# Kernel optimization log

Hardware: AMD Instinct MI355X
Metric: run time of the kernel (lower is better)

Reference implementation:

```python
import jax, jax.numpy as jnp
import numpy as np

B, D, E, K, NC, NH = 8192, 1280, 4, 2, 20, 4
CD = D // NC      # chunk_dim = 64
HD = CD // NH     # head_dim = 16
FF = CD * 4       # ffn hidden = 256
EPS = 1e-8


def setup_inputs() -> dict:
    key = jax.random.key(0)
    ks = jax.random.split(key, 12)
    f = lambda k, sh, s=0.02: jax.random.normal(k, sh, jnp.float32) * s
    return {
        "x": jax.random.normal(ks[0], (B, D), jnp.float32),
        "gate_w1": f(ks[1], (E * 4, D)), "gate_b1": jnp.zeros((E * 4,), jnp.float32),
        "gate_w2": f(ks[2], (E, E * 4)), "gate_b2": jnp.zeros((E,), jnp.float32),
        "pos_embed": f(ks[3], (E, NC, CD)),
        "norm1_g": jnp.ones((E, CD), jnp.float32),
        "in_proj_w": f(ks[4], (E, 3 * CD, CD)), "in_proj_b": jnp.zeros((E, 3 * CD), jnp.float32),
        "out_proj_w": f(ks[5], (E, CD, CD)), "out_proj_b": jnp.zeros((E, CD), jnp.float32),
        "ls1_g": jnp.full((E, CD), 1e-4, jnp.float32),
        "norm2_g": jnp.ones((E, CD), jnp.float32),
        "ffn_w1": f(ks[6], (E, FF, CD)), "ffn_b1": jnp.zeros((E, FF), jnp.float32),
        "ffn_w2": f(ks[7], (E, CD, FF)), "ffn_b2": jnp.zeros((E, CD), jnp.float32),
        "ls2_g": jnp.full((E, CD), 1e-4, jnp.float32),
        "proj_w": f(ks[8], (E, D, D)), "proj_b": jnp.zeros((E, D), jnp.float32),
    }


def _rms(v, g):
    # torch RMSNorm in source: x / (||x||_2 * dim^-0.5 + eps) * g
    n = jnp.linalg.norm(v, axis=-1, keepdims=True) * (CD ** -0.5)
    return v / (n + EPS) * g


def _expert(x, pos, n1g, ipw, ipb, opw, opb, l1, n2g, fw1, fb1, fw2, fb2, l2, pw, pb):
    b = x.shape[0]
    xs = x.reshape(b, NC, CD) + pos            # [b, NC, CD]
    xn = _rms(xs, n1g)
    qkv = xn @ ipw.T + ipb                      # [b, NC, 3*CD]
    q, k, v = jnp.split(qkv, 3, axis=-1)
    q = q.reshape(b, NC, NH, HD).transpose(0, 2, 1, 3)
    k = k.reshape(b, NC, NH, HD).transpose(0, 2, 1, 3)
    v = v.reshape(b, NC, NH, HD).transpose(0, 2, 1, 3)
    att = jax.nn.softmax(jnp.einsum('bhqd,bhkd->bhqk', q, k) * (HD ** -0.5), axis=-1)
    o = jnp.einsum('bhqk,bhkd->bhqd', att, v).transpose(0, 2, 1, 3).reshape(b, NC, CD)
    o = o @ opw.T + opb
    xs = xs + l1 * o                            # residual + LayerScale
    h = jax.nn.relu(_rms(xs, n2g) @ fw1.T + fb1) @ fw2.T + fb2
    xs = xs + l2 * h
    return xs.reshape(b, D) @ pw.T + pb         # final proj [b, D]


def reference(x, gate_w1, gate_b1, gate_w2, gate_b2, pos_embed, norm1_g,
              in_proj_w, in_proj_b, out_proj_w, out_proj_b, ls1_g, norm2_g,
              ffn_w1, ffn_b1, ffn_w2, ffn_b2, ls2_g, proj_w, proj_b):
    logits = jnp.tanh(x @ gate_w1.T + gate_b1) @ gate_w2.T + gate_b2   # [B, E]
    scores = jax.nn.softmax(logits, axis=-1)
    tk_s, tk_i = jax.lax.top_k(scores, K)
    tk_s = tk_s / (tk_s.sum(-1, keepdims=True) + 1e-6)
    onehot = jax.nn.one_hot(tk_i, E, dtype=x.dtype)                    # [B, K, E]
    w = (onehot * tk_s[..., None]).sum(1)                              # [B, E] combine weights
    eout = jax.vmap(_expert, in_axes=(None,) + (0,) * 15)(
        x, pos_embed, norm1_g, in_proj_w, in_proj_b, out_proj_w, out_proj_b,
        ls1_g, norm2_g, ffn_w1, ffn_b1, ffn_w2, ffn_b2, ls2_g, proj_w, proj_b)  # [E, B, D]
    output = jnp.einsum('ebd,be->bd', eout, w)
    aux_loss = jnp.float32(0.0)  # eval mode
    load = onehot.sum((0, 1))    # [E]
    return output, aux_loss, load
```

## Files before the change

### kernel.cpp

```cpp
#include <hip/hip_runtime.h>
#include <hip/hip_bf16.h>
#include <math.h>

#define B_SZ 8192
#define D_SZ 1280
#define NE   4
#define NC   20
#define CD   64
#define NH   4
#define HD   16
#define FF   256

typedef __attribute__((ext_vector_type(8))) short bf16x8;
typedef __attribute__((ext_vector_type(4))) float f32x4;

#define WS_TOPI   256
#define WS_TOPW   (WS_TOPI + 2*B_SZ*4)
#define WS_IDX    (WS_TOPW + 2*B_SZ*4)
#define WS_WGT    (WS_IDX  + 2*B_SZ*4)
#define WS_ER0    (WS_WGT  + 2*B_SZ*4)
#define WS_ER1    (WS_ER0  + B_SZ*4)
#define WS_PRK    (WS_ER1  + B_SZ*4)
#define WS_BBE    (WS_PRK  + B_SZ*4)
#define WS_BBP    (WS_BBE  + 32*4*4)
#define WS_PRA    (WS_BBP  + 32*16*4)
#define WS_PRB    (WS_PRA  + (B_SZ+128)*4)
#define WS_PW1    (WS_PRB  + (B_SZ+128)*4)
#define WS_PW2    (WS_PW1  + (B_SZ+128)*4)
#define WS_PRW    (WS_PW2  + (B_SZ+128)*4)
#define WS_XSF    532480
#define XSF_ROWS  (2*B_SZ + 128)
#define WS_PWB    (WS_XSF + (size_t)XSF_ROWS * D_SZ * 2)
#define WS_IPWB   (WS_PWB  + (size_t)NE * D_SZ * D_SZ * 2)
#define WS_OPWB   (WS_IPWB + (size_t)NE * 192 * 64 * 2)
#define WS_FW1B   (WS_OPWB + (size_t)NE * 64 * 64 * 2)
#define WS_FW2B   (WS_FW1B + (size_t)NE * 256 * 64 * 2)

__global__ __launch_bounds__(256) void convert_pw(const float* __restrict__ pw,
                                                  __hip_bfloat16* __restrict__ pwb)
{
    size_t i = ((size_t)blockIdx.x * 256 + threadIdx.x) * 8;
    float4 a = *(const float4*)(pw + i);
    float4 b = *(const float4*)(pw + i + 4);
    __hip_bfloat16 h[8];
    h[0] = __float2bfloat16(a.x); h[1] = __float2bfloat16(a.y);
    h[2] = __float2bfloat16(a.z); h[3] = __float2bfloat16(a.w);
    h[4] = __float2bfloat16(b.x); h[5] = __float2bfloat16(b.y);
    h[6] = __float2bfloat16(b.z); h[7] = __float2bfloat16(b.w);
    *(uint4*)(pwb + i) = *(uint4*)h;
}

#define N_IPW (NE*192*64)
#define N_OPW (NE*64*64)
#define N_FW1 (NE*256*64)
#define N_FW2 (NE*64*256)
__global__ __launch_bounds__(256) void convert_small(
    const float* __restrict__ ipw, const float* __restrict__ opw,
    const float* __restrict__ fw1, const float* __restrict__ fw2,
    __hip_bfloat16* __restrict__ ipwb, __hip_bfloat16* __restrict__ opwb,
    __hip_bfloat16* __restrict__ fw1b, __hip_bfloat16* __restrict__ fw2b)
{
    size_t i = ((size_t)blockIdx.x * 256 + threadIdx.x) * 8;
    const float* src; __hip_bfloat16* dst; size_t off;
    if (i < N_IPW)                       { src = ipw; dst = ipwb; off = i; }
    else if (i < N_IPW + N_OPW)          { src = opw; dst = opwb; off = i - N_IPW; }
    else if (i < N_IPW + N_OPW + N_FW1)  { src = fw1; dst = fw1b; off = i - N_IPW - N_OPW; }
    else                                 { src = fw2; dst = fw2b; off = i - N_IPW - N_OPW - N_FW1; }
    float4 a = *(const float4*)(src + off);
    float4 b = *(const float4*)(src + off + 4);
    __hip_bfloat16 h[8];
    h[0] = __float2bfloat16(a.x); h[1] = __float2bfloat16(a.y);
    h[2] = __float2bfloat16(a.z); h[3] = __float2bfloat16(a.w);
    h[4] = __float2bfloat16(b.x); h[5] = __float2bfloat16(b.y);
    h[6] = __float2bfloat16(b.z); h[7] = __float2bfloat16(b.w);
    *(uint4*)(dst + off) = *(uint4*)h;
}

__global__ __launch_bounds__(64) void gate_kernel(
    const float* __restrict__ x, const float* __restrict__ gw1, const float* __restrict__ gb1,
    const float* __restrict__ gw2, const float* __restrict__ gb2,
    int* __restrict__ topi, float* __restrict__ topw)
{
    const int b = blockIdx.x;
    const int lane = threadIdx.x;
    float acc[16];
#pragma unroll
    for (int j = 0; j < 16; ++j) acc[j] = 0.f;
    const float* xr = x + (size_t)b * D_SZ;
    for (int t = 0; t < NC; ++t) {
        float xv = xr[t * 64 + lane];
#pragma unroll
        for (int j = 0; j < 16; ++j) acc[j] += xv * gw1[j * D_SZ + t * 64 + lane];
    }
#pragma unroll
    for (int j = 0; j < 16; ++j) {
        acc[j] += __shfl_xor(acc[j], 32, 64);
        acc[j] += __shfl_xor(acc[j], 16, 64);
        acc[j] += __shfl_xor(acc[j], 8, 64);
        acc[j] += __shfl_xor(acc[j], 4, 64);
        acc[j] += __shfl_xor(acc[j], 2, 64);
        acc[j] += __shfl_xor(acc[j], 1, 64);
    }
    if (lane == 0) {
        float h[16];
#pragma unroll
        for (int j = 0; j < 16; ++j) h[j] = tanhf(acc[j] + gb1[j]);
        float l[4];
#pragma unroll
        for (int e = 0; e < 4; ++e) {
            float sv = gb2[e];
#pragma unroll
            for (int j = 0; j < 16; ++j) sv += h[j] * gw2[e * 16 + j];
            l[e] = sv;
        }
        float m = fmaxf(fmaxf(l[0], l[1]), fmaxf(l[2], l[3]));
        float p[4];
        float sum = 0.f;
#pragma unroll
        for (int e = 0; e < 4; ++e) { p[e] = expf(l[e] - m); sum += p[e]; }
#pragma unroll
        for (int e = 0; e < 4; ++e) p[e] /= sum;
        int i1 = 0;
#pragma unroll
        for (int e = 1; e < 4; ++e) if (p[e] > p[i1]) i1 = e;
        int i2 = (i1 == 0) ? 1 : 0;
#pragma unroll
        for (int e = 0; e < 4; ++e) if (e != i1 && p[e] > p[i2]) i2 = e;
        float s1 = p[i1], s2 = p[i2];
        float denom = s1 + s2 + 1e-6f;
        topi[b * 2 + 0] = i1;
        topi[b * 2 + 1] = i2;
        topw[b * 2 + 0] = s1 / denom;
        topw[b * 2 + 1] = s2 / denom;
    }
}

__global__ __launch_bounds__(256) void count_kernel(
    const int* __restrict__ topi,
    int* __restrict__ cnt, int* __restrict__ pcnt,
    int* __restrict__ er0, int* __restrict__ er1, int* __restrict__ prk,
    int* __restrict__ bbe, int* __restrict__ bbp)
{
    __shared__ int he[4], hp[16];
    const int t = threadIdx.x;
    const int blk = blockIdx.x;
    const int b = blk * 256 + t;
    if (t < 4) he[t] = 0;
    if (t < 16) hp[t] = 0;
    __syncthreads();
    int e0 = topi[b * 2], e1 = topi[b * 2 + 1];
    er0[b] = atomicAdd(&he[e0], 1);
    er1[b] = atomicAdd(&he[e1], 1);
    prk[b] = atomicAdd(&hp[e0 * 4 + e1], 1);
    __syncthreads();
    if (t < 4)  bbe[blk * 4 + t]  = atomicAdd(&cnt[t], he[t]);
    if (t < 16) bbp[blk * 16 + t] = atomicAdd(&pcnt[t], hp[t]);
}

__global__ void offsets_kernel(const int* __restrict__ cnt, const int* __restrict__ pcnt,
                               int* __restrict__ offA, int* __restrict__ poff,
                               float* __restrict__ load_out)
{
    if (threadIdx.x == 0 && blockIdx.x == 0) {
        int a = 0;
#pragma unroll
        for (int e = 0; e < 4; ++e) { offA[e] = a; a += cnt[e]; }
        offA[4] = a;
        int q = 0;
#pragma unroll
        for (int p = 0; p < 16; ++p) { poff[p] = q; q += pcnt[p]; }
        poff[16] = q;
#pragma unroll
        for (int e = 0; e < 4; ++e) load_out[e] = (float)cnt[e];
    }
}

__global__ __launch_bounds__(256) void fill_kernel(
    const int* __restrict__ topi, const float* __restrict__ topw,
    const int* __restrict__ offA, const int* __restrict__ poff,
    const int* __restrict__ er0, const int* __restrict__ er1, const int* __restrict__ prk,
    const int* __restrict__ bbe, const int* __restrict__ bbp,
    int* __restrict__ idx_list, float* __restrict__ wgt_list,
    int* __restrict__ prA, int* __restrict__ prB,
    float* __restrict__ pw1, float* __restrict__ pw2, int* __restrict__ prow)
{
    const int b = blockIdx.x * 256 + threadIdx.x;
    const int blk = blockIdx.x;
    int e0 = topi[b * 2], e1 = topi[b * 2 + 1];
    float w0 = topw[b * 2], w1 = topw[b * 2 + 1];
    int slot0 = offA[e0] + bbe[blk * 4 + e0] + er0[b];
    int slot1 = offA[e1] + bbe[blk * 4 + e1] + er1[b];
    idx_list[slot0] = b; wgt_list[slot0] = w0;
    idx_list[slot1] = b; wgt_list[slot1] = w1;
    int p = e0 * 4 + e1;
    int pos = poff[p] + bbp[blk * 16 + p] + prk[b];
    prA[pos] = slot0; prB[pos] = slot1;
    pw1[pos] = w0; pw2[pos] = w1; prow[pos] = b;
}

__global__ __launch_bounds__(256, 6) void expert_inner(
    const float* __restrict__ x, const float* __restrict__ pos,
    const float* __restrict__ n1g,
    const __hip_bfloat16* __restrict__ ipwb, const float* __restrict__ ipb,
    const __hip_bfloat16* __restrict__ opwb, const float* __restrict__ opb,
    const float* __restrict__ ls1, const float* __restrict__ n2g,
    const __hip_bfloat16* __restrict__ fw1b, const float* __restrict__ fb1,
    const __hip_bfloat16* __restrict__ fw2b, const float* __restrict__ fb2,
    const float* __restrict__ ls2,
    const int* __restrict__ offA, const int* __restrict__ idx_list,
    const float* __restrict__ wgt_list,
    __hip_bfloat16* __restrict__ xsf)
{
    __shared__ float xs[NC][66];
    __shared__ __hip_bfloat16 xnb[32][72];
    __shared__ __hip_bfloat16 ovl[32 * 260];

    __hip_bfloat16 (* const qkb)[136] = (__hip_bfloat16(*)[136])ovl;
    __hip_bfloat16 (* const vtb)[40]  = (__hip_bfloat16(*)[40])(ovl + 32*136);
    __hip_bfloat16 (* const h1b)[260] = (__hip_bfloat16(*)[260])ovl;

    const int t = threadIdx.x;
    const int w = t >> 6;
    const int lane = t & 63;
    const int l15 = lane & 15, lg = lane >> 4;
    const int s = blockIdx.x;
    const int e = (s >= offA[1]) + (s >= offA[2]) + (s >= offA[3]);
    const int b = idx_list[s];
    const float wgt = wgt_list[s];

    {
        float g = n1g[e * CD + lane];
        const float* xr = x + (size_t)b * D_SZ;
        const float* pr = pos + (size_t)e * D_SZ;
#pragma unroll
        for (int ic = 0; ic < 5; ++ic) {
            int c = w * 5 + ic;
            float v = xr[c * 64 + lane] + pr[c * 64 + lane];
            xs[c][lane] = v;
            float ss = v * v;
            ss += __shfl_xor(ss, 32, 64); ss += __shfl_xor(ss, 16, 64);
            ss += __shfl_xor(ss, 8, 64);  ss += __shfl_xor(ss, 4, 64);
            ss += __shfl_xor(ss, 2, 64);  ss += __shfl_xor(ss, 1, 64);
            float n = sqrtf(ss) * 0.125f + 1e-8f;
            xnb[c][lane] = __float2bfloat16(v * __builtin_amdgcn_rcpf(n) * g);
        }
        __hip_bfloat16 z = __float2bfloat16(0.f);
        for (int i = t; i < 12 * 64; i += 256) xnb[20 + (i >> 6)][i & 63] = z;
    }
    __syncthreads();

    {
        bf16x8 af[2][2];
#pragma unroll
        for (int mt = 0; mt < 2; ++mt)
#pragma unroll
            for (int ks = 0; ks < 2; ++ks)
                af[mt][ks] = *(const bf16x8*)&xnb[mt * 16 + l15][ks * 32 + lg * 8];
#pragma unroll
        for (int i = 0; i < 3; ++i) {
            int tn = w * 3 + i;
            int n = tn * 16 + l15;
            f32x4 acc[2] = {{0,0,0,0},{0,0,0,0}};
#pragma unroll
            for (int ks = 0; ks < 2; ++ks) {
                bf16x8 bf = *(const bf16x8*)(ipwb + ((size_t)(e * 192 + n)) * 64 + ks * 32 + lg * 8);
#pragma unroll
                for (int mt = 0; mt < 2; ++mt)
                    acc[mt] = __builtin_amdgcn_mfma_f32_16x16x32_bf16(af[mt][ks], bf, acc[mt], 0, 0, 0);
            }
            float bias = ipb[e * 192 + n];
            if (tn < 8) {
#pragma unroll
                for (int mt = 0; mt < 2; ++mt)
#pragma unroll
                    for (int r = 0; r < 4; ++r)
                        qkb[mt * 16 + lg * 4 + r][n] = __float2bfloat16(acc[mt][r] + bias);
            } else {
#pragma unroll
                for (int mt = 0; mt < 2; ++mt)
#pragma unroll
                    for (int r = 0; r < 4; ++r)
                        vtb[n - 128][mt * 16 + lg * 4 + r] = __float2bfloat16(acc[mt][r] + bias);
            }
        }
    }
    __syncthreads();

    {
        bf16x8 zf = {0,0,0,0,0,0,0,0};
        bf16x8 aq[2], bk[2];
#pragma unroll
        for (int mt = 0; mt < 2; ++mt)
            aq[mt] = (lg < 2) ? *(const bf16x8*)&qkb[mt * 16 + l15][w * 16 + lg * 8] : zf;
#pragma unroll
        for (int nt = 0; nt < 2; ++nt)
            bk[nt] = (lg < 2) ? *(const bf16x8*)&qkb[nt * 16 + l15][64 + w * 16 + lg * 8] : zf;
        bf16x8 bv = *(const bf16x8*)&vtb[w * 16 + l15][lg * 8];
        __syncthreads();

        f32x4 sacc[2][2];
#pragma unroll
        for (int mt = 0; mt < 2; ++mt)
#pragma unroll
            for (int nt = 0; nt < 2; ++nt)
                sacc[mt][nt] = __builtin_amdgcn_mfma_f32_16x16x32_bf16(
                    aq[mt], bk[nt], (f32x4){0,0,0,0}, 0, 0, 0);

#pragma unroll
        for (int mt = 0; mt < 2; ++mt) {
#pragma unroll
            for (int r = 0; r < 4; ++r) {
                float e0 = __expf(sacc[mt][0][r] * 0.25f);
                float e1 = (l15 < 4) ? __expf(sacc[mt][1][r] * 0.25f) : 0.f;
                float sm = e0 + e1;
                sm += __shfl_xor(sm, 1, 64);
                sm += __shfl_xor(sm, 2, 64);
                sm += __shfl_xor(sm, 4, 64);
                sm += __shfl_xor(sm, 8, 64);
                float is = __builtin_amdgcn_rcpf(sm);
                int qi = mt * 16 + lg * 4 + r;
                qkb[qi][w * 32 + l15]      = __float2bfloat16(e0 * is);
                qkb[qi][w * 32 + 16 + l15] = __float2bfloat16(e1 * is);
            }
        }
#pragma unroll
        for (int mt = 0; mt < 2; ++mt) {
            bf16x8 ap = *(const bf16x8*)&qkb[mt * 16 + l15][w * 32 + lg * 8];
            f32x4 oacc = __builtin_amdgcn_mfma_f32_16x16x32_bf16(ap, bv, (f32x4){0,0,0,0}, 0, 0, 0);
#pragma unroll
            for (int r = 0; r < 4; ++r)
                xnb[mt * 16 + lg * 4 + r][w * 16 + l15] = __float2bfloat16(oacc[r]);
        }
    }
    __syncthreads();

    {
        bf16x8 af[2][2];
#pragma unroll
        for (int mt = 0; mt < 2; ++mt)
#pragma unroll
            for (int ks = 0; ks < 2; ++ks)
                af[mt][ks] = *(const bf16x8*)&xnb[mt * 16 + l15][ks * 32 + lg * 8];
        int n = w * 16 + l15;
        f32x4 acc[2] = {{0,0,0,0},{0,0,0,0}};
#pragma unroll
        for (int ks = 0; ks < 2; ++ks) {
            bf16x8 bf = *(const bf16x8*)(opwb + ((size_t)(e * 64 + n)) * 64 + ks * 32 + lg * 8);
#pragma unroll
            for (int mt = 0; mt < 2; ++mt)
                acc[mt] = __builtin_amdgcn_mfma_f32_16x16x32_bf16(af[mt][ks], bf, acc[mt], 0, 0, 0);
        }
        float l1v = ls1[e * 64 + n], ob = opb[e * 64 + n];
#pragma unroll
        for (int mt = 0; mt < 2; ++mt)
#pragma unroll
            for (int r = 0; r < 4; ++r) {
                int m = mt * 16 + lg * 4 + r;
                if (m < NC) xs[m][n] += l1v * (acc[mt][r] + ob);
            }
    }
    __syncthreads();

    {
        float g = n2g[e * CD + lane];
#pragma unroll
        for (int ic = 0; ic < 5; ++ic) {
            int c = w * 5 + ic;
            float v = xs[c][lane];
            float ss = v * v;
            ss += __shfl_xor(ss, 32, 64); ss += __shfl_xor(ss, 16, 64);
            ss += __shfl_xor(ss, 8, 64);  ss += __shfl_xor(ss, 4, 64);
            ss += __shfl_xor(ss, 2, 64);  ss += __shfl_xor(ss, 1, 64);
            float n = sqrtf(ss) * 0.125f + 1e-8f;
            xnb[c][lane] = __float2bfloat16(v * __builtin_amdgcn_rcpf(n) * g);
        }
    }
    __syncthreads();

    {
        bf16x8 af[2][2];
#pragma unroll
        for (int mt = 0; mt < 2; ++mt)
#pragma unroll
            for (int ks = 0; ks < 2; ++ks)
                af[mt][ks] = *(const bf16x8*)&xnb[mt * 16 + l15][ks * 32 + lg * 8];
#pragma unroll
        for (int i = 0; i < 4; ++i) {
            int n = (w * 4 + i) * 16 + l15;
            f32x4 acc[2] = {{0,0,0,0},{0,0,0,0}};
#pragma unroll
            for (int ks = 0; ks < 2; ++ks) {
                bf16x8 bf = *(const bf16x8*)(fw1b + ((size_t)(e * 256 + n)) * 64 + ks * 32 + lg * 8);
#pragma unroll
                for (int mt = 0; mt < 2; ++mt)
                    acc[mt] = __builtin_amdgcn_mfma_f32_16x16x32_bf16(af[mt][ks], bf, acc[mt], 0, 0, 0);
            }
            float b1 = fb1[e * 256 + n];
#pragma unroll
            for (int mt = 0; mt < 2; ++mt)
#pragma unroll
                for (int r = 0; r < 4; ++r)
                    h1b[mt * 16 + lg * 4 + r][n] = __float2bfloat16(fmaxf(acc[mt][r] + b1, 0.f));
        }
    }
    __syncthreads();

    {
        int n = w * 16 + l15;
        f32x4 acc[2] = {{0,0,0,0},{0,0,0,0}};
#pragma unroll
        for (int ks = 0; ks < 8; ++ks) {
            bf16x8 bf = *(const bf16x8*)(fw2b + ((size_t)(e * 64 + n)) * 256 + ks * 32 + lg * 8);
#pragma unroll
            for (int mt = 0; mt < 2; ++mt) {
                bf16x8 af = *(const bf16x8*)&h1b[mt * 16 + l15][ks * 32 + lg * 8];
                acc[mt] = __builtin_amdgcn_mfma_f32_16x16x32_bf16(af, bf, acc[mt], 0, 0, 0);
            }
        }
        float l2v = ls2[e * 64 + n], b2 = fb2[e * 64 + n];
#pragma unroll
        for (int mt = 0; mt < 2; ++mt)
#pragma unroll
            for (int r = 0; r < 4; ++r) {
                int m = mt * 16 + lg * 4 + r;
                if (m < NC) xs[m][n] += l2v * (acc[mt][r] + b2);
            }
    }
    __syncthreads();

    for (int idx = t; idx < D_SZ; idx += 256)
        xsf[(size_t)s * D_SZ + idx] = __float2bfloat16(wgt * xs[idx >> 6][idx & 63]);
}

#define PROWP 130

__global__ __launch_bounds__(256) void proj_pair(
    const __hip_bfloat16* __restrict__ xsf, const __hip_bfloat16* __restrict__ pwb,
    const float* __restrict__ pb, const int* __restrict__ poff,
    const int* __restrict__ prA, const int* __restrict__ prB,
    const float* __restrict__ pw1, const float* __restrict__ pw2,
    const int* __restrict__ prow, float* __restrict__ out)
{
    __shared__ short As[8][PROWP][8];
    __shared__ short Bs[8][PROWP][8];
    __shared__ int   sSlot[2][128];
    __shared__ float sW[2][128];
    __shared__ int   sRow[128];

    int mblk = blockIdx.x;
    int p = 0, base = 0, M = 0;
#pragma unroll
    for (int pp = 0; pp < 16; ++pp) {
        int b0 = poff[pp], b1 = poff[pp + 1];
        int nb = (b1 - b0 + 127) >> 7;
        if (p == pp && mblk >= nb) { mblk -= nb; p = pp + 1; }
        else if (p == pp) { base = b0; M = b1 - b0; }
    }
    if (p >= 16) return;
    const int ea = p >> 2, eb = p & 3;

    const int m0 = mblk * 128;
    const int n0 = blockIdx.y * 128;
    const int t = threadIdx.x;
    const int w = t >> 6, lane = t & 63;
    const int wm = (w & 1) * 64, wn = (w >> 1) * 64;
    const int l15 = lane & 15, lg = lane >> 4;

    if (t < 128) {
        int posn = base + m0 + t;
        int sa = prA[posn], sb = prB[posn];
        sSlot[0][t] = min(max(sa, 0), 2 * B_SZ);
        sSlot[1][t] = min(max(sb, 0), 2 * B_SZ);
        sW[0][t] = pw1[posn]; sW[1][t] = pw2[posn];
        sRow[t] = prow[posn];
    }
    __syncthreads();

    f32x4 acc[4][4];
#pragma unroll
    for (int i = 0; i < 4; ++i)
#pragma unroll
        for (int j = 0; j < 4; ++j) acc[i][j] = (f32x4){0.f, 0.f, 0.f, 0.f};

    const int arow0 = t >> 3;
    const int akb = t & 7;

#pragma unroll
    for (int ph = 0; ph < 2; ++ph) {
        const __hip_bfloat16* Bg = pwb + (size_t)(ph ? eb : ea) * D_SZ * D_SZ + (size_t)n0 * D_SZ;
        int aslot[4];
#pragma unroll
        for (int i = 0; i < 4; ++i) aslot[i] = sSlot[ph][arow0 + 32 * i];

        for (int kt = 0; kt < D_SZ; kt += 64) {
            __syncthreads();
#pragma unroll
            for (int i = 0; i < 4; ++i) {
                int row = arow0 + 32 * i;
                *(uint4*)&As[akb][row][0] =
                    *(const uint4*)(xsf + (size_t)aslot[i] * D_SZ + kt + akb * 8);
                *(uint4*)&Bs[akb][row][0] =
                    *(const uint4*)(Bg + (size_t)row * D_SZ + kt + akb * 8);
            }
            __syncthreads();
#pragma unroll
            for (int ks = 0; ks < 2; ++ks) {
                int kb = ks * 4 + lg;
                bf16x8 af[4], bfr[4];
#pragma unroll
                for (int ti = 0; ti < 4; ++ti) af[ti]  = *(const bf16x8*)&As[kb][wm + ti * 16 + l15][0];
#pragma unroll
                for (int tj = 0; tj < 4; ++tj) bfr[tj] = *(const bf16x8*)&Bs[kb][wn + tj * 16 + l15][0];
#pragma unroll
                for (int ti = 0; ti < 4; ++ti)
#pragma unroll
                    for (int tj = 0; tj < 4; ++tj)
                        acc[ti][tj] = __builtin_amdgcn_mfma_f32_16x16x32_bf16(
                            af[ti], bfr[tj], acc[ti][tj], 0, 0, 0);
            }
        }
    }

    float pbva[4], pbvb[4];
#pragma unroll
    for (int tj = 0; tj < 4; ++tj) {
        int nc = n0 + wn + tj * 16 + l15;
        pbva[tj] = pb[(size_t)ea * D_SZ + nc];
        pbvb[tj] = pb[(size_t)eb * D_SZ + nc];
    }

#pragma unroll
    for (int ti = 0; ti < 4; ++ti) {
#pragma unroll
        for (int r = 0; r < 4; ++r) {
            int m = wm + ti * 16 + lg * 4 + r;
            if (m0 + m < M) {
                float w1 = sW[0][m], w2 = sW[1][m];
                float* orow = out + (size_t)sRow[m] * D_SZ + n0 + wn + l15;
#pragma unroll
                for (int tj = 0; tj < 4; ++tj)
                    orow[tj * 16] = acc[ti][tj][r] + w1 * pbva[tj] + w2 * pbvb[tj];
            }
        }
    }
}

extern "C" void kernel_launch(void* const* d_in, const int* in_sizes, int n_in,
                              void* d_out, int out_size, void* d_ws, size_t ws_size,
                              hipStream_t stream)
{
    const float* x   = (const float*)d_in[0];
    const float* gw1 = (const float*)d_in[1];
    const float* gb1 = (const float*)d_in[2];
    const float* gw2 = (const float*)d_in[3];
    const float* gb2 = (const float*)d_in[4];
    const float* pos = (const float*)d_in[5];
    const float* n1g = (const float*)d_in[6];
    const float* ipw = (const float*)d_in[7];
    const float* ipb = (const float*)d_in[8];
    const float* opw = (const float*)d_in[9];
    const float* opb = (const float*)d_in[10];
    const float* ls1 = (const float*)d_in[11];
    const float* n2g = (const float*)d_in[12];
    const float* fw1 = (const float*)d_in[13];
    const float* fb1 = (const float*)d_in[14];
    const float* fw2 = (const float*)d_in[15];
    const float* fb2 = (const float*)d_in[16];
    const float* ls2 = (const float*)d_in[17];
    const float* pw  = (const float*)d_in[18];
    const float* pb  = (const float*)d_in[19];

    float* out = (float*)d_out;

    char* ws = (char*)d_ws;
    int*   cnt      = (int*)(ws + 0);
    int*   pcnt     = (int*)(ws + 16);
    int*   offA     = (int*)(ws + 80);
    int*   poff     = (int*)(ws + 112);
    int*   topi     = (int*)(ws + WS_TOPI);
    float* topw     = (float*)(ws + WS_TOPW);
    int*   idx_list = (int*)(ws + WS_IDX);
    float* wgt_list = (float*)(ws + WS_WGT);
    int*   er0      = (int*)(ws + WS_ER0);
    int*   er1      = (int*)(ws + WS_ER1);
    int*   prk      = (int*)(ws + WS_PRK);
    int*   bbe      = (int*)(ws + WS_BBE);
    int*   bbp      = (int*)(ws + WS_BBP);
    int*   prA      = (int*)(ws + WS_PRA);
    int*   prB      = (int*)(ws + WS_PRB);
    float* pw1      = (float*)(ws + WS_PW1);
    float* pw2      = (float*)(ws + WS_PW2);
    int*   prow     = (int*)(ws + WS_PRW);
    __hip_bfloat16* xsf  = (__hip_bfloat16*)(ws + WS_XSF);
    __hip_bfloat16* pwb  = (__hip_bfloat16*)(ws + WS_PWB);
    __hip_bfloat16* ipwb = (__hip_bfloat16*)(ws + WS_IPWB);
    __hip_bfloat16* opwb = (__hip_bfloat16*)(ws + WS_OPWB);
    __hip_bfloat16* fw1b = (__hip_bfloat16*)(ws + WS_FW1B);
    __hip_bfloat16* fw2b = (__hip_bfloat16*)(ws + WS_FW2B);

    hipMemsetAsync(d_ws, 0, 256, stream);
    hipMemsetAsync(out + (size_t)B_SZ * D_SZ, 0, 5 * sizeof(float), stream);

    float* load_out = out + (size_t)B_SZ * D_SZ + 1;

    convert_pw<<<NE * D_SZ * D_SZ / (256 * 8), 256, 0, stream>>>(pw, pwb);
    convert_small<<<(N_IPW + N_OPW + N_FW1 + N_FW2) / (256 * 8), 256, 0, stream>>>(
        ipw, opw, fw1, fw2, ipwb, opwb, fw1b, fw2b);
    gate_kernel<<<B_SZ, 64, 0, stream>>>(x, gw1, gb1, gw2, gb2, topi, topw);
    count_kernel<<<B_SZ / 256, 256, 0, stream>>>(topi, cnt, pcnt, er0, er1, prk, bbe, bbp);
    offsets_kernel<<<1, 64, 0, stream>>>(cnt, pcnt, offA, poff, load_out);
    fill_kernel<<<B_SZ / 256, 256, 0, stream>>>(topi, topw, offA, poff, er0, er1, prk,
                                                bbe, bbp, idx_list, wgt_list,
                                                prA, prB, pw1, pw2, prow);
    expert_inner<<<2 * B_SZ, 256, 0, stream>>>(x, pos, n1g, ipwb, ipb, opwb, opb, ls1,
                                               n2g, fw1b, fb1, fw2b, fb2, ls2,
                                               offA, idx_list, wgt_list, xsf);
    proj_pair<<<dim3(96, D_SZ / 128), 256, 0, stream>>>(
        xsf, pwb, pb, poff, prA, prB, pw1, pw2, prow, out);
}
```

Measured before the change: 557.4 us.

## Process one token-expert slot per wavefront instead of per workgroup in expert_inner

Restructures expert_inner so each 64-lane wavefront independently handles one (token, expert) slot, with four slots per 256-thread block. Per-wave LDS regions and register-resident residual state replace the shared xs array, so every __syncthreads becomes a wave-local lgkmcnt wait. Attention runs one head at a time, and the FFN is chunked over the hidden dimension so the second GEMM accumulates in registers. The goal is to remove block-wide barrier stalls and idle waves in the small per-token GEMMs. In exchange each wave does 4x more sequential MFMA work, register pressure rises (launch bounds lowered to 3), and weight reloads per wave increase.

Measured after the change: 529.2 us. 5.1% less time.

```diff
diff --git a/kernel.cpp b/kernel.cpp
--- a/kernel.cpp
+++ b/kernel.cpp
@@ -13,6 +13,9 @@
 
 typedef __attribute__((ext_vector_type(8))) short bf16x8;
 typedef __attribute__((ext_vector_type(4))) float f32x4;
+
+#define WFENCE() do { asm volatile("s_waitcnt lgkmcnt(0)" ::: "memory"); \
+                      __builtin_amdgcn_sched_barrier(0); } while (0)
 
 #define WS_TOPI   256
 #define WS_TOPW   (WS_TOPI + 2*B_SZ*4)
@@ -198,7 +201,7 @@
     pw1[pos] = w0; pw2[pos] = w1; prow[pos] = b;
 }
 
-__global__ __launch_bounds__(256, 6) void expert_inner(
+__global__ __launch_bounds__(256, 3) void expert_inner(
     const float* __restrict__ x, const float* __restrict__ pos,
     const float* __restrict__ n1g,
     const __hip_bfloat16* __restrict__ ipwb, const float* __restrict__ ipb,
@@ -211,225 +214,264 @@
     const float* __restrict__ wgt_list,
     __hip_bfloat16* __restrict__ xsf)
 {
-    __shared__ float xs[NC][66];
-    __shared__ __hip_bfloat16 xnb[32][72];
-    __shared__ __hip_bfloat16 ovl[32 * 260];
-
-    __hip_bfloat16 (* const qkb)[136] = (__hip_bfloat16(*)[136])ovl;
-    __hip_bfloat16 (* const vtb)[40]  = (__hip_bfloat16(*)[40])(ovl + 32*136);
-    __hip_bfloat16 (* const h1b)[260] = (__hip_bfloat16(*)[260])ovl;
+    __shared__ __hip_bfloat16 s_big[4][32][72];
+    __shared__ __hip_bfloat16 s_mid[4][32][40];
+    __shared__ __hip_bfloat16 s_vt [4][16][40];
 
     const int t = threadIdx.x;
     const int w = t >> 6;
     const int lane = t & 63;
     const int l15 = lane & 15, lg = lane >> 4;
-    const int s = blockIdx.x;
+    const int s = blockIdx.x * 4 + w;
     const int e = (s >= offA[1]) + (s >= offA[2]) + (s >= offA[3]);
     const int b = idx_list[s];
     const float wgt = wgt_list[s];
 
+    __hip_bfloat16 (* const big)[72] = s_big[w];
+    __hip_bfloat16 (* const mid)[40] = s_mid[w];
+    __hip_bfloat16 (* const vt)[40]  = s_vt[w];
+
+    const float* xg = x + (size_t)b * D_SZ;
+    const float* pg = pos + (size_t)e * D_SZ;
+
+    f32x4 xsr[2][4];
+
     {
-        float g = n1g[e * CD + lane];
-        const float* xr = x + (size_t)b * D_SZ;
-        const float* pr = pos + (size_t)e * D_SZ;
-#pragma unroll
-        for (int ic = 0; ic < 5; ++ic) {
-            int c = w * 5 + ic;
-            float v = xr[c * 64 + lane] + pr[c * 64 + lane];
-            xs[c][lane] = v;
-            float ss = v * v;
-            ss += __shfl_xor(ss, 32, 64); ss += __shfl_xor(ss, 16, 64);
-            ss += __shfl_xor(ss, 8, 64);  ss += __shfl_xor(ss, 4, 64);
-            ss += __shfl_xor(ss, 2, 64);  ss += __shfl_xor(ss, 1, 64);
-            float n = sqrtf(ss) * 0.125f + 1e-8f;
-            xnb[c][lane] = __float2bfloat16(v * __builtin_amdgcn_rcpf(n) * g);
-        }
-        __hip_bfloat16 z = __float2bfloat16(0.f);
-        for (int i = t; i < 12 * 64; i += 256) xnb[20 + (i >> 6)][i & 63] = z;
-    }
-    __syncthreads();
+        float g1[4];
+#pragma unroll
+        for (int nt = 0; nt < 4; ++nt) g1[nt] = n1g[e * CD + nt * 16 + l15];
+#pragma unroll
+        for (int mt = 0; mt < 2; ++mt)
+#pragma unroll
+            for (int r = 0; r < 4; ++r) {
+                const int row = mt * 16 + lg * 4 + r;
+                float ss = 0.f;
+#pragma unroll
+                for (int nt = 0; nt < 4; ++nt) {
+                    float v = 0.f;
+                    if (row < NC) v = xg[row * 64 + nt * 16 + l15] + pg[row * 64 + nt * 16 + l15];
+                    xsr[mt][nt][r] = v;
+                    ss += v * v;
+                }
+                ss += __shfl_xor(ss, 1); ss += __shfl_xor(ss, 2);
+                ss += __shfl_xor(ss, 4); ss += __shfl_xor(ss, 8);
+                float inv = __builtin_amdgcn_rcpf(sqrtf(ss) * 0.125f + 1e-8f);
+#pragma unroll
+                for (int nt = 0; nt < 4; ++nt)
+                    big[row][nt * 16 + l15] = __float2bfloat16(xsr[mt][nt][r] * inv * g1[nt]);
+            }
+    }
+    WFENCE();
+
+    bf16x8 af[2][2];
+#pragma unroll
+    for (int mt = 0; mt < 2; ++mt)
+#pragma unroll
+        for (int ks = 0; ks < 2; ++ks)
+            af[mt][ks] = *(const bf16x8*)&big[mt * 16 + l15][ks * 32 + lg * 8];
+
+    for (int h = 0; h < NH; ++h) {
+        f32x4 qa[2], ka[2], va[2];
+#pragma unroll
+        for (int mt = 0; mt < 2; ++mt) { qa[mt] = (f32x4){0,0,0,0}; ka[mt] = (f32x4){0,0,0,0}; va[mt] = (f32x4){0,0,0,0}; }
+        const int nq = h * 16 + l15;
+#pragma unroll
+        for (int ks = 0; ks < 2; ++ks) {
+            bf16x8 bq = *(const bf16x8*)(ipwb + ((size_t)(e * 192 + nq)) * 64 + ks * 32 + lg * 8);
+            bf16x8 bk_ = *(const bf16x8*)(ipwb + ((size_t)(e * 192 + 64 + nq)) * 64 + ks * 32 + lg * 8);
+            bf16x8 bv_ = *(const bf16x8*)(ipwb + ((size_t)(e * 192 + 128 + nq)) * 64 + ks * 32 + lg * 8);
+#pragma unroll
+            for (int mt = 0; mt < 2; ++mt) {
+                qa[mt] = __builtin_amdgcn_mfma_f32_16x16x32_bf16(af[mt][ks], bq, qa[mt], 0, 0, 0);
+                ka[mt] = __builtin_amdgcn_mfma_f32_16x16x32_bf16(af[mt][ks], bk_, ka[mt], 0, 0, 0);
+                va[mt] = __builtin_amdgcn_mfma_f32_16x16x32_bf16(af[mt][ks], bv_, va[mt], 0, 0, 0);
+            }
+        }
+        const float biq = ipb[e * 192 + nq];
+        const float bik = ipb[e * 192 + 64 + nq];
+        const float biv = ipb[e * 192 + 128 + nq];
+#pragma unroll
+        for (int mt = 0; mt < 2; ++mt)
+#pragma unroll
+            for (int r = 0; r < 4; ++r) {
+                const int row = mt * 16 + lg * 4 + r;
+                mid[row][l15]      = __float2bfloat16(qa[mt][r] + biq);
+                mid[row][16 + l15] = __float2bfloat16(ka[mt][r] + bik);
+                vt[l15][row]       = __float2bfloat16(va[mt][r] + biv);
+            }
+        WFENCE();
+
+        bf16x8 aq[2], bk[2], bv;
+        const bf16x8 zf = {0,0,0,0,0,0,0,0};
+#pragma unroll
+        for (int mt = 0; mt < 2; ++mt) {
+            aq[mt] = zf;
+            if (lg < 2) aq[mt] = *(const bf16x8*)&mid[mt * 16 + l15][lg * 8];
+        }
+#pragma unroll
+        for (int nt = 0; nt < 2; ++nt) {
+            bk[nt] = zf;
+            if (lg < 2) bk[nt] = *(const bf16x8*)&mid[nt * 16 + l15][16 + lg * 8];
+        }
+        bv = *(const bf16x8*)&vt[l15][lg * 8];
+
+        f32x4 sc[2][2];
+#pragma unroll
+        for (int mt = 0; mt < 2; ++mt)
+#pragma unroll
+            for (int nt = 0; nt < 2; ++nt)
+                sc[mt][nt] = __builtin_amdgcn_mfma_f32_16x16x32_bf16(aq[mt], bk[nt], (f32x4){0,0,0,0}, 0, 0, 0);
+
+#pragma unroll
+        for (int mt = 0; mt < 2; ++mt)
+#pragma unroll
+            for (int r = 0; r < 4; ++r) {
+                float e0 = __expf(sc[mt][0][r] * 0.25f);
+                float e1 = (l15 < 4) ? __expf(sc[mt][1][r] * 0.25f) : 0.f;
+                float sm = e0 + e1;
+                sm += __shfl_xor(sm, 1); sm += __shfl_xor(sm, 2);
+                sm += __shfl_xor(sm, 4); sm += __shfl_xor(sm, 8);
+                float is = __builtin_amdgcn_rcpf(sm);
+                const int row = mt * 16 + lg * 4 + r;
+                mid[row][l15]      = __float2bfloat16(e0 * is);
+                mid[row][16 + l15] = __float2bfloat16((l15 < 4) ? e1 * is : 0.f);
+            }
+        WFENCE();
+
+#pragma unroll
+        for (int mt = 0; mt < 2; ++mt) {
+            bf16x8 ap = *(const bf16x8*)&mid[mt * 16 + l15][lg * 8];
+            f32x4 o = __builtin_amdgcn_mfma_f32_16x16x32_bf16(ap, bv, (f32x4){0,0,0,0}, 0, 0, 0);
+#pragma unroll
+            for (int r = 0; r < 4; ++r)
+                big[mt * 16 + lg * 4 + r][h * 16 + l15] = __float2bfloat16(o[r]);
+        }
+        WFENCE();
+    }
 
     {
-        bf16x8 af[2][2];
+        bf16x8 aO[2][2];
 #pragma unroll
         for (int mt = 0; mt < 2; ++mt)
 #pragma unroll
             for (int ks = 0; ks < 2; ++ks)
-                af[mt][ks] = *(const bf16x8*)&xnb[mt * 16 + l15][ks * 32 + lg * 8];
-#pragma unroll
-        for (int i = 0; i < 3; ++i) {
-            int tn = w * 3 + i;
-            int n = tn * 16 + l15;
-            f32x4 acc[2] = {{0,0,0,0},{0,0,0,0}};
+                aO[mt][ks] = *(const bf16x8*)&big[mt * 16 + l15][ks * 32 + lg * 8];
+#pragma unroll
+        for (int nt = 0; nt < 4; ++nt) {
+            const int n = nt * 16 + l15;
+            f32x4 po[2] = {{0,0,0,0},{0,0,0,0}};
 #pragma unroll
             for (int ks = 0; ks < 2; ++ks) {
-                bf16x8 bf = *(const bf16x8*)(ipwb + ((size_t)(e * 192 + n)) * 64 + ks * 32 + lg * 8);
+                bf16x8 bw = *(const bf16x8*)(opwb + ((size_t)(e * 64 + n)) * 64 + ks * 32 + lg * 8);
 #pragma unroll
                 for (int mt = 0; mt < 2; ++mt)
-                    acc[mt] = __builtin_amdgcn_mfma_f32_16x16x32_bf16(af[mt][ks], bf, acc[mt], 0, 0, 0);
-            }
-            float bias = ipb[e * 192 + n];
-            if (tn < 8) {
+                    po[mt] = __builtin_amdgcn_mfma_f32_16x16x32_bf16(aO[mt][ks], bw, po[mt], 0, 0, 0);
+            }
+            const float lv = ls1[e * 64 + n], ob = opb[e * 64 + n];
+#pragma unroll
+            for (int mt = 0; mt < 2; ++mt)
+#pragma unroll
+                for (int r = 0; r < 4; ++r)
+                    xsr[mt][nt][r] += lv * (po[mt][r] + ob);
+        }
+    }
+
+    {
+        float g2[4];
+#pragma unroll
+        for (int nt = 0; nt < 4; ++nt) g2[nt] = n2g[e * CD + nt * 16 + l15];
+#pragma unroll
+        for (int mt = 0; mt < 2; ++mt)
+#pragma unroll
+            for (int r = 0; r < 4; ++r) {
+                const int row = mt * 16 + lg * 4 + r;
+                float ss = 0.f;
+#pragma unroll
+                for (int nt = 0; nt < 4; ++nt) ss += xsr[mt][nt][r] * xsr[mt][nt][r];
+                ss += __shfl_xor(ss, 1); ss += __shfl_xor(ss, 2);
+                ss += __shfl_xor(ss, 4); ss += __shfl_xor(ss, 8);
+                float inv = __builtin_amdgcn_rcpf(sqrtf(ss) * 0.125f + 1e-8f);
+#pragma unroll
+                for (int nt = 0; nt < 4; ++nt)
+                    big[row][nt * 16 + l15] = __float2bfloat16(xsr[mt][nt][r] * inv * g2[nt]);
+            }
+    }
+    WFENCE();
+
+    {
+        bf16x8 af2[2][2];
+#pragma unroll
+        for (int mt = 0; mt < 2; ++mt)
+#pragma unroll
+            for (int ks = 0; ks < 2; ++ks)
+                af2[mt][ks] = *(const bf16x8*)&big[mt * 16 + l15][ks * 32 + lg * 8];
+
+        f32x4 a2[2][4];
+#pragma unroll
+        for (int mt = 0; mt < 2; ++mt)
+#pragma unroll
+            for (int nt = 0; nt < 4; ++nt) a2[mt][nt] = (f32x4){0,0,0,0};
+
+        for (int c = 0; c < 8; ++c) {
+#pragma unroll
+            for (int ntc = 0; ntc < 2; ++ntc) {
+                const int n = c * 32 + ntc * 16 + l15;
+                f32x4 hc[2] = {{0,0,0,0},{0,0,0,0}};
+#pragma unroll
+                for (int ks = 0; ks < 2; ++ks) {
+                    bf16x8 bw = *(const bf16x8*)(fw1b + ((size_t)(e * 256 + n)) * 64 + ks * 32 + lg * 8);
+#pragma unroll
+                    for (int mt = 0; mt < 2; ++mt)
+                        hc[mt] = __builtin_amdgcn_mfma_f32_16x16x32_bf16(af2[mt][ks], bw, hc[mt], 0, 0, 0);
+                }
+                const float b1 = fb1[e * 256 + n];
 #pragma unroll
                 for (int mt = 0; mt < 2; ++mt)
 #pragma unroll
                     for (int r = 0; r < 4; ++r)
-                        qkb[mt * 16 + lg * 4 + r][n] = __float2bfloat16(acc[mt][r] + bias);
-            } else {
+                        mid[mt * 16 + lg * 4 + r][ntc * 16 + l15] =
+                            __float2bfloat16(fmaxf(hc[mt][r] + b1, 0.f));
+            }
+            WFENCE();
+            bf16x8 ah[2];
+#pragma unroll
+            for (int mt = 0; mt < 2; ++mt)
+                ah[mt] = *(const bf16x8*)&mid[mt * 16 + l15][lg * 8];
+#pragma unroll
+            for (int nt = 0; nt < 4; ++nt) {
+                const int n = nt * 16 + l15;
+                bf16x8 bw2 = *(const bf16x8*)(fw2b + ((size_t)(e * 64 + n)) * 256 + c * 32 + lg * 8);
 #pragma unroll
                 for (int mt = 0; mt < 2; ++mt)
-#pragma unroll
-                    for (int r = 0; r < 4; ++r)
-                        vtb[n - 128][mt * 16 + lg * 4 + r] = __float2bfloat16(acc[mt][r] + bias);
-            }
-        }
-    }
-    __syncthreads();
-
-    {
-        bf16x8 zf = {0,0,0,0,0,0,0,0};
-        bf16x8 aq[2], bk[2];
-#pragma unroll
-        for (int mt = 0; mt < 2; ++mt)
-            aq[mt] = (lg < 2) ? *(const bf16x8*)&qkb[mt * 16 + l15][w * 16 + lg * 8] : zf;
-#pragma unroll
-        for (int nt = 0; nt < 2; ++nt)
-            bk[nt] = (lg < 2) ? *(const bf16x8*)&qkb[nt * 16 + l15][64 + w * 16 + lg * 8] : zf;
-        bf16x8 bv = *(const bf16x8*)&vtb[w * 16 + l15][lg * 8];
-        __syncthreads();
-
-        f32x4 sacc[2][2];
-#pragma unroll
-        for (int mt = 0; mt < 2; ++mt)
-#pragma unroll
-            for (int nt = 0; nt < 2; ++nt)
-                sacc[mt][nt] = __builtin_amdgcn_mfma_f32_16x16x32_bf16(
-                    aq[mt], bk[nt], (f32x4){0,0,0,0}, 0, 0, 0);
-
-#pragma unroll
-        for (int mt = 0; mt < 2; ++mt) {
-#pragma unroll
-            for (int r = 0; r < 4; ++r) {
-                float e0 = __expf(sacc[mt][0][r] * 0.25f);
-                float e1 = (l15 < 4) ? __expf(sacc[mt][1][r] * 0.25f) : 0.f;
-                float sm = e0 + e1;
-                sm += __shfl_xor(sm, 1, 64);
-                sm += __shfl_xor(sm, 2, 64);
-                sm += __shfl_xor(sm, 4, 64);
-                sm += __shfl_xor(sm, 8, 64);
-                float is = __builtin_amdgcn_rcpf(sm);
-                int qi = mt * 16 + lg * 4 + r;
-                qkb[qi][w * 32 + l15]      = __float2bfloat16(e0 * is);
-                qkb[qi][w * 32 + 16 + l15] = __float2bfloat16(e1 * is);
-            }
-        }
-#pragma unroll
-        for (int mt = 0; mt < 2; ++mt) {
-            bf16x8 ap = *(const bf16x8*)&qkb[mt * 16 + l15][w * 32 + lg * 8];
-            f32x4 oacc = __builtin_amdgcn_mfma_f32_16x16x32_bf16(ap, bv, (f32x4){0,0,0,0}, 0, 0, 0);
-#pragma unroll
-            for (int r = 0; r < 4; ++r)
-                xnb[mt * 16 + lg * 4 + r][w * 16 + l15] = __float2bfloat16(oacc[r]);
-        }
-    }
-    __syncthreads();
-
-    {
-        bf16x8 af[2][2];
-#pragma unroll
-        for (int mt = 0; mt < 2; ++mt)
-#pragma unroll
-            for (int ks = 0; ks < 2; ++ks)
-                af[mt][ks] = *(const bf16x8*)&xnb[mt * 16 + l15][ks * 32 + lg * 8];
-        int n = w * 16 + l15;
-        f32x4 acc[2] = {{0,0,0,0},{0,0,0,0}};
-#pragma unroll
-        for (int ks = 0; ks < 2; ++ks) {
-            bf16x8 bf = *(const bf16x8*)(opwb + ((size_t)(e * 64 + n)) * 64 + ks * 32 + lg * 8);
+                    a2[mt][nt] = __builtin_amdgcn_mfma_f32_16x16x32_bf16(ah[mt], bw2, a2[mt][nt], 0, 0, 0);
+            }
+            WFENCE();
+        }
+
+#pragma unroll
+        for (int nt = 0; nt < 4; ++nt) {
+            const int n = nt * 16 + l15;
+            const float lv = ls2[e * 64 + n], b2 = fb2[e * 64 + n];
 #pragma unroll
             for (int mt = 0; mt < 2; ++mt)
-                acc[mt] = __builtin_amdgcn_mfma_f32_16x16x32_bf16(af[mt][ks], bf, acc[mt], 0, 0, 0);
-        }
-        float l1v = ls1[e * 64 + n], ob = opb[e * 64 + n];
-#pragma unroll
-        for (int mt = 0; mt < 2; ++mt)
-#pragma unroll
-            for (int r = 0; r < 4; ++r) {
-                int m = mt * 16 + lg * 4 + r;
-                if (m < NC) xs[m][n] += l1v * (acc[mt][r] + ob);
-            }
-    }
-    __syncthreads();
-
-    {
-        float g = n2g[e * CD + lane];
-#pragma unroll
-        for (int ic = 0; ic < 5; ++ic) {
-            int c = w * 5 + ic;
-            float v = xs[c][lane];
-            float ss = v * v;
-            ss += __shfl_xor(ss, 32, 64); ss += __shfl_xor(ss, 16, 64);
-            ss += __shfl_xor(ss, 8, 64);  ss += __shfl_xor(ss, 4, 64);
-            ss += __shfl_xor(ss, 2, 64);  ss += __shfl_xor(ss, 1, 64);
-            float n = sqrtf(ss) * 0.125f + 1e-8f;
-            xnb[c][lane] = __float2bfloat16(v * __builtin_amdgcn_rcpf(n) * g);
-        }
-    }
-    __syncthreads();
-
-    {
-        bf16x8 af[2][2];
-#pragma unroll
-        for (int mt = 0; mt < 2; ++mt)
-#pragma unroll
-            for (int ks = 0; ks < 2; ++ks)
-                af[mt][ks] = *(const bf16x8*)&xnb[mt * 16 + l15][ks * 32 + lg * 8];
-#pragma unroll
-        for (int i = 0; i < 4; ++i) {
-            int n = (w * 4 + i) * 16 + l15;
-            f32x4 acc[2] = {{0,0,0,0},{0,0,0,0}};
-#pragma unroll
-            for (int ks = 0; ks < 2; ++ks) {
-                bf16x8 bf = *(const bf16x8*)(fw1b + ((size_t)(e * 256 + n)) * 64 + ks * 32 + lg * 8);
-#pragma unroll
-                for (int mt = 0; mt < 2; ++mt)
-                    acc[mt] = __builtin_amdgcn_mfma_f32_16x16x32_bf16(af[mt][ks], bf, acc[mt], 0, 0, 0);
-            }
-            float b1 = fb1[e * 256 + n];
-#pragma unroll
-            for (int mt = 0; mt < 2; ++mt)
 #pragma unroll
                 for (int r = 0; r < 4; ++r)
-                    h1b[mt * 16 + lg * 4 + r][n] = __float2bfloat16(fmaxf(acc[mt][r] + b1, 0.f));
-        }
-    }
-    __syncthreads();
-
-    {
-        int n = w * 16 + l15;
-        f32x4 acc[2] = {{0,0,0,0},{0,0,0,0}};
-#pragma unroll
-        for (int ks = 0; ks < 8; ++ks) {
-            bf16x8 bf = *(const bf16x8*)(fw2b + ((size_t)(e * 64 + n)) * 256 + ks * 32 + lg * 8);
-#pragma unroll
-            for (int mt = 0; mt < 2; ++mt) {
-                bf16x8 af = *(const bf16x8*)&h1b[mt * 16 + l15][ks * 32 + lg * 8];
-                acc[mt] = __builtin_amdgcn_mfma_f32_16x16x32_bf16(af, bf, acc[mt], 0, 0, 0);
-            }
-        }
-        float l2v = ls2[e * 64 + n], b2 = fb2[e * 64 + n];
-#pragma unroll
-        for (int mt = 0; mt < 2; ++mt)
-#pragma unroll
-            for (int r = 0; r < 4; ++r) {
-                int m = mt * 16 + lg * 4 + r;
-                if (m < NC) xs[m][n] += l2v * (acc[mt][r] + b2);
-            }
-    }
-    __syncthreads();
-
-    for (int idx = t; idx < D_SZ; idx += 256)
-        xsf[(size_t)s * D_SZ + idx] = __float2bfloat16(wgt * xs[idx >> 6][idx & 63]);
+                    xsr[mt][nt][r] += lv * (a2[mt][nt][r] + b2);
+        }
+    }
+
+#pragma unroll
+    for (int mt = 0; mt < 2; ++mt)
+#pragma unroll
+        for (int r = 0; r < 4; ++r) {
+            const int row = mt * 16 + lg * 4 + r;
+            if (row < NC) {
+#pragma unroll
+                for (int nt = 0; nt < 4; ++nt)
+                    xsf[(size_t)s * D_SZ + row * 64 + nt * 16 + l15] =
+                        __float2bfloat16(wgt * xsr[mt][nt][r]);
+            }
+        }
 }
 
 #define PROWP 130
@@ -612,9 +654,9 @@
     fill_kernel<<<B_SZ / 256, 256, 0, stream>>>(topi, topw, offA, poff, er0, er1, prk,
                                                 bbe, bbp, idx_list, wgt_list,
                                                 prA, prB, pw1, pw2, prow);
-    expert_inner<<<2 * B_SZ, 256, 0, stream>>>(x, pos, n1g, ipwb, ipb, opwb, opb, ls1,
-                                               n2g, fw1b, fb1, fw2b, fb2, ls2,
-                                               offA, idx_list, wgt_list, xsf);
+    expert_inner<<<(2 * B_SZ) / 4, 256, 0, stream>>>(x, pos, n1g, ipwb, ipb, opwb, opb, ls1,
+                                                     n2g, fw1b, fb1, fw2b, fb2, ls2,
+                                                     offA, idx_list, wgt_list, xsf);
     proj_pair<<<dim3(96, D_SZ / 128), 256, 0, stream>>>(
         xsf, pwb, pb, poff, prA, prB, pw1, pw2, prow, out);
 }
```
